# Optimization experiments

Hardware: AMD Instinct MI355X
Metric: run time of the kernel (lower is better)

Reference implementation:

```python
import jax, jax.numpy as jnp
import numpy as np

NEG_SLOPE = 0.2

def gat_conv(x, edge_index, W, a_src, a_dst, b, heads, out_ch, concat):
    # PyG GATConv with add_self_loops=True, LeakyReLU(0.2) attention.
    N = x.shape[0]
    loop = jnp.arange(N, dtype=edge_index.dtype)
    src = jnp.concatenate([edge_index[0], loop])  # source nodes j
    dst = jnp.concatenate([edge_index[1], loop])  # target nodes i
    h = (x @ W).reshape(N, heads, out_ch)                      # [N,H,C]
    alpha_src = jnp.sum(h * a_src[None], axis=-1)              # [N,H]
    alpha_dst = jnp.sum(h * a_dst[None], axis=-1)              # [N,H]
    e = alpha_src[src] + alpha_dst[dst]                        # [E,H]
    e = jax.nn.leaky_relu(e, NEG_SLOPE)
    # per-destination segment softmax (self-loops guarantee every segment non-empty)
    emax = jax.ops.segment_max(e, dst, num_segments=N)         # [N,H]
    ez = jnp.exp(e - emax[dst])
    denom = jax.ops.segment_sum(ez, dst, num_segments=N)       # [N,H]
    alpha = ez / denom[dst]                                    # [E,H]
    msg = h[src] * alpha[:, :, None]                           # [E,H,C]
    out = jax.ops.segment_sum(msg, dst, num_segments=N)        # [N,H,C]
    out = out.reshape(N, heads * out_ch) if concat else out.mean(axis=1)
    return out + b


def setup_inputs() -> dict:
    key = jax.random.key(0)
    ks = jax.random.split(key, 10)
    N, E = 100000, 3200000
    x = jax.random.normal(ks[0], (N, 7), dtype=jnp.float32)
    edge_index = jax.random.randint(ks[1], (2, E), 0, N, dtype=jnp.int32)
    W1 = jax.random.normal(ks[2], (7, 64), dtype=jnp.float32) * 0.3
    a_src1 = jax.random.normal(ks[3], (4, 16), dtype=jnp.float32) * 0.3
    a_dst1 = jax.random.normal(ks[4], (4, 16), dtype=jnp.float32) * 0.3
    b1 = jax.random.normal(ks[5], (64,), dtype=jnp.float32) * 0.1
    W2 = jax.random.normal(ks[6], (64, 6), dtype=jnp.float32) * 0.15
    a_src2 = jax.random.normal(ks[7], (1, 6), dtype=jnp.float32) * 0.3
    a_dst2 = jax.random.normal(ks[8], (1, 6), dtype=jnp.float32) * 0.3
    b2 = jax.random.normal(ks[9], (6,), dtype=jnp.float32) * 0.1
    return {"x": x, "edge_index": edge_index, "W1": W1, "a_src1": a_src1,
            "a_dst1": a_dst1, "b1": b1, "W2": W2, "a_src2": a_src2,
            "a_dst2": a_dst2, "b2": b2}


def reference(x, edge_index, W1, a_src1, a_dst1, b1, W2, a_src2, a_dst2, b2):
    h = gat_conv(x, edge_index, W1, a_src1, a_dst1, b1, heads=4, out_ch=16, concat=True)
    h = jax.nn.elu(h)
    h = gat_conv(h, edge_index, W2, a_src2, a_dst2, b2, heads=1, out_ch=6, concat=True)
    return jax.nn.log_softmax(h, axis=1)
```

## Files before the change

kernel.cpp:

```cpp
#include <hip/hip_runtime.h>
#include <math.h>

#define NEG_SLOPE 0.2f

__device__ __forceinline__ float lrelu(float x) { return x > 0.f ? x : NEG_SLOPE * x; }

__device__ __forceinline__ unsigned encf(float f) {
    unsigned u = __float_as_uint(f);
    return (u & 0x80000000u) ? ~u : (u | 0x80000000u);
}
__device__ __forceinline__ float decf(unsigned u) {
    return __uint_as_float((u & 0x80000000u) ? (u ^ 0x80000000u) : ~u);
}

__global__ void __launch_bounds__(512)
phaseAH(const float* __restrict__ x, const float* __restrict__ W1,
        const float* __restrict__ a_src, const float* __restrict__ a_dst,
        const int* __restrict__ dst,
        float* __restrict__ xa, float* __restrict__ adst1,
        float* __restrict__ eloop1,
        int* __restrict__ counts, unsigned* __restrict__ gmax1,
        int N, int E, int nbuck) {
    __shared__ int hist[1024];
    __shared__ unsigned bmax1[4];
    int tid = threadIdx.x;
    for (int j = tid; j < nbuck; j += 512) hist[j] = 0;
    if (tid < 4) bmax1[tid] = 0u;
    __syncthreads();

    int per = (E + gridDim.x - 1) / gridDim.x;
    int i0 = blockIdx.x * per, i1 = min(E, i0 + per);
    for (int i = i0 + tid; i < i1; i += 512)
        atomicAdd(&hist[dst[i] >> 7], 1);

    int npb = (N + gridDim.x - 1) / gridDim.x;
    int n0 = blockIdx.x * npb, n1 = min(N, n0 + npb);
    int lane = tid & 63;
    int head = lane >> 4, c = lane & 15;
    for (int node = n0 + (tid >> 6); node < n1; node += 8) {
        float h = 0.f;
        #pragma unroll
        for (int k = 0; k < 7; k++) h += x[node * 7 + k] * W1[k * 64 + lane];

        float s = h * a_src[lane];
        float d = h * a_dst[lane];
        #pragma unroll
        for (int m = 8; m >= 1; m >>= 1) {
            s += __shfl_xor(s, m);
            d += __shfl_xor(d, m);
        }
        if (lane < 7) xa[(size_t)node * 12 + lane] = x[node * 7 + lane];
        if (c == 0) {
            xa[(size_t)node * 12 + 7 + head] = s;
            adst1[node * 4 + head] = d;
            eloop1[node * 4 + head] = lrelu(s + d);
            atomicMax(&bmax1[head], encf(s));
        }
    }
    __syncthreads();
    for (int j = tid; j < nbuck; j += 512)
        counts[j * gridDim.x + blockIdx.x] = hist[j];
    if (tid < 4) atomicMax(&gmax1[tid], bmax1[tid]);
}

__global__ void scan1(const int* __restrict__ in, int* __restrict__ outv,
                      int* __restrict__ blockSum, int n) {
    __shared__ int sm[256];
    int tid = threadIdx.x;
    int i = blockIdx.x * 256 + tid;
    int v = (i < n) ? in[i] : 0;
    sm[tid] = v;
    __syncthreads();
    for (int off = 1; off < 256; off <<= 1) {
        int t = sm[tid];
        int add = (tid >= off) ? sm[tid - off] : 0;
        __syncthreads();
        sm[tid] = t + add;
        __syncthreads();
    }
    if (i < n) outv[i] = sm[tid] - v;
    if (tid == 255) blockSum[blockIdx.x] = sm[255];
}

__global__ void scan2(int* __restrict__ blockSum, int nb) {
    __shared__ int sm[1024];
    int tid = threadIdx.x;
    int v = (tid < nb) ? blockSum[tid] : 0;
    sm[tid] = v;
    __syncthreads();
    for (int off = 1; off < 1024; off <<= 1) {
        int t = sm[tid];
        int add = (tid >= off) ? sm[tid - off] : 0;
        __syncthreads();
        sm[tid] = t + add;
        __syncthreads();
    }
    if (tid < nb) blockSum[tid] = sm[tid] - v;
}

__global__ void scatterS(const int* __restrict__ src, const int* __restrict__ dst,
                         const int* __restrict__ ocounts, const int* __restrict__ blockSum,
                         int* __restrict__ ebuf, int E, int nbuck) {
    __shared__ int cur[1024];
    for (int j = threadIdx.x; j < nbuck; j += blockDim.x) {
        int idx = j * gridDim.x + blockIdx.x;
        cur[j] = ocounts[idx] + blockSum[idx >> 8];
    }
    __syncthreads();
    int per = (E + gridDim.x - 1) / gridDim.x;
    int i0 = blockIdx.x * per, i1 = min(E, i0 + per);
    for (int i = i0 + threadIdx.x; i < i1; i += blockDim.x) {
        int d = dst[i];
        int b = d >> 7;
        int pos = atomicAdd(&cur[b], 1);
        ebuf[pos] = src[i] | ((d & 127) << 17);
    }
}

__global__ void __launch_bounds__(512, 2)
fusedG1(const int* __restrict__ ebuf, const int* __restrict__ ocounts,
        const int* __restrict__ blockSum, const unsigned* __restrict__ gmax1,
        const float* __restrict__ xa, const float* __restrict__ adst1,
        const float* __restrict__ eloop1,
        const float* __restrict__ W1, const float* __restrict__ b1,
        const float* __restrict__ W2,
        const float* __restrict__ a_src2, const float* __restrict__ a_dst2,
        int* __restrict__ rowstart, int* __restrict__ deg, int* __restrict__ csr,
        float* __restrict__ h2pad, float* __restrict__ asrc2,
        float* __restrict__ adst2, float* __restrict__ eloop2,
        unsigned* __restrict__ gmax2, int N, int E, int G, int nbuck) {
    int b = blockIdx.x;
    int idxb = b * G;
    int beg = ocounts[idxb] + blockSum[idxb >> 8];
    int end = E;
    if (b + 1 < nbuck) {
        int idx2 = (b + 1) * G;
        end = ocounts[idx2] + blockSum[idx2 >> 8];
    }
    int base = b << 7;
    int tid = threadIdx.x;

    __shared__ int cnt[128], sc[128], rloc[128], lcur[128];
    __shared__ float W1s[448], W2s[384], b1s[64];
    __shared__ unsigned bmax2s;

    if (tid == 0) bmax2s = 0u;
    if (tid < 128) cnt[tid] = 0;
    for (int j = tid; j < 448; j += 512) W1s[j] = W1[j];
    for (int j = tid; j < 384; j += 512) W2s[j] = W2[j];
    if (tid < 64) b1s[tid] = b1[tid];
    __syncthreads();
    for (int i = beg + tid; i < end; i += 512)
        atomicAdd(&cnt[ebuf[i] >> 17], 1);
    __syncthreads();
    if (tid < 128) sc[tid] = cnt[tid];
    __syncthreads();
    for (int off = 1; off < 128; off <<= 1) {
        int t = (tid < 128) ? sc[tid] : 0;
        int add = (tid >= off && tid < 128) ? sc[tid - off] : 0;
        __syncthreads();
        if (tid < 128) sc[tid] = t + add;
        __syncthreads();
    }
    if (tid < 128) {
        int ex = sc[tid] - cnt[tid];
        rloc[tid] = beg + ex;
        lcur[tid] = 0;
        int node = base + tid;
        if (node < N) { rowstart[node] = beg + ex; deg[node] = cnt[tid]; }
    }
    __syncthreads();
    for (int i = beg + tid; i < end; i += 512) {
        int e = ebuf[i];
        int j = e >> 17;
        int pos = atomicAdd(&lcur[j], 1);
        csr[rloc[j] + pos] = e & 0x1FFFF;
    }
    __syncthreads();

    int g = tid >> 2, h = tid & 3;
    int node = base + g;
    if (node < N) {
        int grs = rloc[g], dg = cnt[g];
        float adh = adst1[node * 4 + h];
        float m = lrelu(decf(gmax1[h]) + adh);
        float z0 = __expf(eloop1[node * 4 + h] - m);
        float den = z0;

        const float4* xav = (const float4*)xa;
        float4 S0 = xav[(size_t)node * 3];
        float4 S1 = xav[(size_t)node * 3 + 1];
        float xc0 = z0 * S0.x, xc1 = z0 * S0.y, xc2 = z0 * S0.z, xc3 = z0 * S0.w;
        float xc4 = z0 * S1.x, xc5 = z0 * S1.y, xc6 = z0 * S1.z;

        if (dg > 0) {
            int iB = (dg > 1) ? 1 : 0;
            int sA = csr[grs];
            int sB = csr[grs + iB];
            float4 A0 = xav[(size_t)sA * 3], A1 = xav[(size_t)sA * 3 + 1], A2 = xav[(size_t)sA * 3 + 2];
            float4 B0 = xav[(size_t)sB * 3], B1 = xav[(size_t)sB * 3 + 1], B2 = xav[(size_t)sB * 3 + 2];
            for (int k = 0; k < dg; ++k) {
                int k2 = (k + 2 < dg) ? k + 2 : dg - 1;
                int sC = csr[grs + k2];
                float4 C0 = xav[(size_t)sC * 3], C1 = xav[(size_t)sC * 3 + 1], C2 = xav[(size_t)sC * 3 + 2];
                float av = (h == 0) ? A1.w : (h == 1) ? A2.x : (h == 2) ? A2.y : A2.z;
                float z = __expf(lrelu(av + adh) - m);
                den += z;
                xc0 = fmaf(z, A0.x, xc0); xc1 = fmaf(z, A0.y, xc1);
                xc2 = fmaf(z, A0.z, xc2); xc3 = fmaf(z, A0.w, xc3);
                xc4 = fmaf(z, A1.x, xc4); xc5 = fmaf(z, A1.y, xc5);
                xc6 = fmaf(z, A1.z, xc6);
                A0 = B0; A1 = B1; A2 = B2;
                B0 = C0; B1 = C1; B2 = C2;
            }
        }

        float inv = 1.f / den;
        float xv0 = xc0 * inv, xv1 = xc1 * inv, xv2 = xc2 * inv, xv3 = xc3 * inv;
        float xv4 = xc4 * inv, xv5 = xc5 * inv, xv6 = xc6 * inv;
        float hh[6] = {0.f, 0.f, 0.f, 0.f, 0.f, 0.f};
        #pragma unroll
        for (int c = 0; c < 16; ++c) {
            int ch = h * 16 + c;
            const float* Wc = &W1s[ch];
            float v = xv0 * Wc[0] + xv1 * Wc[64] + xv2 * Wc[128] + xv3 * Wc[192]
                    + xv4 * Wc[256] + xv5 * Wc[320] + xv6 * Wc[384] + b1s[ch];
            v = v > 0.f ? v : __expf(v) - 1.f;
            const float* W2c = &W2s[ch * 6];
            #pragma unroll
            for (int c2 = 0; c2 < 6; ++c2) hh[c2] = fmaf(v, W2c[c2], hh[c2]);
        }
        #pragma unroll
        for (int c2 = 0; c2 < 6; ++c2) {
            hh[c2] += __shfl_xor(hh[c2], 1);
            hh[c2] += __shfl_xor(hh[c2], 2);
        }
        float as = 0.f, ad = 0.f;
        #pragma unroll
        for (int c2 = 0; c2 < 6; ++c2) {
            as += hh[c2] * a_src2[c2];
            ad += hh[c2] * a_dst2[c2];
        }
        if (h == 0) {
            #pragma unroll
            for (int c2 = 0; c2 < 6; ++c2) h2pad[(size_t)node * 8 + c2] = hh[c2];
            h2pad[(size_t)node * 8 + 6] = as;
            asrc2[node] = as;
            adst2[node] = ad;
            eloop2[node] = lrelu(as + ad);
            atomicMax(&bmax2s, encf(as));
        }
    }
    __syncthreads();
    if (tid == 0) atomicMax(gmax2, bmax2s);
}

__global__ void gatherL2(const int* __restrict__ csr, const int* __restrict__ rowstart,
                         const int* __restrict__ deg, const unsigned* __restrict__ gmax2,
                         const float* __restrict__ h2pad, const float* __restrict__ adst2,
                         const float* __restrict__ eloop2,
                         const float* __restrict__ b2, float* __restrict__ out, int N) {
    int node = blockIdx.x * 8 + (threadIdx.x >> 5);
    if (node >= N) return;
    int lane = threadIdx.x & 31;
    int rs = rowstart[node], ke = rs + deg[node];

    float adn = adst2[node];
    float m = lrelu(decf(*gmax2) + adn);

    float den = 0.f;
    float a0 = 0.f, a1 = 0.f, a2 = 0.f, a3 = 0.f, a4 = 0.f, a5 = 0.f;
    if (lane == 0) {
        float z0 = __expf(eloop2[node] - m);
        den = z0;
        float4 lo = ((const float4*)h2pad)[(size_t)node * 2];
        float4 hi = ((const float4*)h2pad)[(size_t)node * 2 + 1];
        a0 = z0 * lo.x; a1 = z0 * lo.y; a2 = z0 * lo.z;
        a3 = z0 * lo.w; a4 = z0 * hi.x; a5 = z0 * hi.y;
    }
    for (int k = rs + lane; k < ke; k += 32) {
        int s = csr[k];
        float4 lo = ((const float4*)h2pad)[(size_t)s * 2];
        float4 hi = ((const float4*)h2pad)[(size_t)s * 2 + 1];
        float z = __expf(lrelu(hi.z + adn) - m);
        den += z;
        a0 = fmaf(z, lo.x, a0); a1 = fmaf(z, lo.y, a1); a2 = fmaf(z, lo.z, a2);
        a3 = fmaf(z, lo.w, a3); a4 = fmaf(z, hi.x, a4); a5 = fmaf(z, hi.y, a5);
    }
    #pragma unroll
    for (int mm = 16; mm >= 1; mm >>= 1) {
        den += __shfl_xor(den, mm);
        a0 += __shfl_xor(a0, mm); a1 += __shfl_xor(a1, mm); a2 += __shfl_xor(a2, mm);
        a3 += __shfl_xor(a3, mm); a4 += __shfl_xor(a4, mm); a5 += __shfl_xor(a5, mm);
    }
    if (lane == 0) {
        float inv = 1.f / den;
        float v[6] = { a0 * inv + b2[0], a1 * inv + b2[1], a2 * inv + b2[2],
                       a3 * inv + b2[3], a4 * inv + b2[4], a5 * inv + b2[5] };
        float mxv = -1e30f;
        #pragma unroll
        for (int cc = 0; cc < 6; cc++) mxv = fmaxf(mxv, v[cc]);
        float ssum = 0.f;
        #pragma unroll
        for (int cc = 0; cc < 6; cc++) ssum += __expf(v[cc] - mxv);
        float lse = mxv + logf(ssum);
        #pragma unroll
        for (int cc = 0; cc < 6; cc++) out[node * 6 + cc] = v[cc] - lse;
    }
}

extern "C" void kernel_launch(void* const* d_in, const int* in_sizes, int n_in,
                              void* d_out, int out_size, void* d_ws, size_t ws_size,
                              hipStream_t stream) {
    const float* x      = (const float*)d_in[0];
    const int*   ei     = (const int*)d_in[1];
    const float* W1     = (const float*)d_in[2];
    const float* a_src1 = (const float*)d_in[3];
    const float* a_dst1 = (const float*)d_in[4];
    const float* b1     = (const float*)d_in[5];
    const float* W2     = (const float*)d_in[6];
    const float* a_src2 = (const float*)d_in[7];
    const float* a_dst2 = (const float*)d_in[8];
    const float* b2     = (const float*)d_in[9];
    float* out = (float*)d_out;

    const int N = in_sizes[0] / 7;
    const int E = in_sizes[1] / 2;
    const int* src = ei;
    const int* dst = ei + E;
    const int nbuck = (N + 127) >> 7;
    const int G = 256;
    const int M = nbuck * G;

    float* w = (float*)d_ws;
    float* xa     = w;  w += (size_t)N * 12;
    float* adst1  = w;  w += (size_t)N * 4;
    float* eloop1 = w;  w += (size_t)N * 4;
    float* h2pad  = w;  w += (size_t)N * 8;
    float* asrc2  = w;  w += (size_t)N;
    float* adst2  = w;  w += (size_t)N;
    float* eloop2 = w;  w += (size_t)N;
    int* ip = (int*)w;
    int* ebuf     = ip; ip += E;
    int* deg      = ip; ip += N;
    int* rowstart = ip; ip += N;
    int* blockSum = ip; ip += 1024;
    int* csr      = ip; ip += E;
    int* counts   = ip; ip += M;
    int* ocounts  = ip; ip += M;
    unsigned* gmax1 = (unsigned*)ip; ip += 4;
    unsigned* gmax2 = (unsigned*)ip; ip += 4;

    int nbM = (M + 255) / 256;

    hipMemsetAsync(gmax1, 0, 8 * sizeof(unsigned), stream);
    phaseAH<<<dim3(G), 512, 0, stream>>>(x, W1, a_src1, a_dst1, dst,
                                         xa, adst1, eloop1,
                                         counts, gmax1, N, E, nbuck);
    scan1<<<dim3(nbM), 256, 0, stream>>>(counts, ocounts, blockSum, M);
    scan2<<<1, 1024, 0, stream>>>(blockSum, nbM);
    scatterS<<<dim3(G), 512, 0, stream>>>(src, dst, ocounts, blockSum, ebuf, E, nbuck);
    fusedG1<<<dim3(nbuck), 512, 0, stream>>>(ebuf, ocounts, blockSum, gmax1,
                                             xa, adst1, eloop1,
                                             W1, b1, W2, a_src2, a_dst2,
                                             rowstart, deg, csr,
                                             h2pad, asrc2, adst2, eloop2,
                                             gmax2, N, E, G, nbuck);
    gatherL2<<<dim3((N + 7) / 8), 256, 0, stream>>>(csr, rowstart, deg, gmax2,
                                                    h2pad, adst2, eloop2, b2, out, N);
}
```

Measured before the change: 210.9 us.

## Widen dst buckets to 256 nodes and assign two heads per thread in fusedG1

Destination buckets now cover 256 nodes instead of 128, which halves the number of fusedG1 blocks and of histogram/scatter bins. In fusedG1 each thread now handles two attention heads for one node instead of one, so each gathered neighbour row of xa is loaded by half as many threads. This trades more registers per thread (two sets of accumulators) and a serial loop over twice as many edges per block for less redundant gather traffic. The blockSum indexing is simplified to blockSum[b], which relies on G equal to 256.

```diff
diff --git a/kernel.cpp b/kernel.cpp
--- a/kernel.cpp
+++ b/kernel.cpp
@@ -21,7 +21,7 @@
         float* __restrict__ eloop1,
         int* __restrict__ counts, unsigned* __restrict__ gmax1,
         int N, int E, int nbuck) {
-    __shared__ int hist[1024];
+    __shared__ int hist[512];
     __shared__ unsigned bmax1[4];
     int tid = threadIdx.x;
     for (int j = tid; j < nbuck; j += 512) hist[j] = 0;
@@ -31,7 +31,7 @@
     int per = (E + gridDim.x - 1) / gridDim.x;
     int i0 = blockIdx.x * per, i1 = min(E, i0 + per);
     for (int i = i0 + tid; i < i1; i += 512)
-        atomicAdd(&hist[dst[i] >> 7], 1);
+        atomicAdd(&hist[dst[i] >> 8], 1);
 
     int npb = (N + gridDim.x - 1) / gridDim.x;
     int n0 = blockIdx.x * npb, n1 = min(N, n0 + npb);
@@ -101,7 +101,7 @@
 __global__ void scatterS(const int* __restrict__ src, const int* __restrict__ dst,
                          const int* __restrict__ ocounts, const int* __restrict__ blockSum,
                          int* __restrict__ ebuf, int E, int nbuck) {
-    __shared__ int cur[1024];
+    __shared__ int cur[512];
     for (int j = threadIdx.x; j < nbuck; j += blockDim.x) {
         int idx = j * gridDim.x + blockIdx.x;
         cur[j] = ocounts[idx] + blockSum[idx >> 8];
@@ -111,9 +111,9 @@
     int i0 = blockIdx.x * per, i1 = min(E, i0 + per);
     for (int i = i0 + threadIdx.x; i < i1; i += blockDim.x) {
         int d = dst[i];
-        int b = d >> 7;
+        int b = d >> 8;
         int pos = atomicAdd(&cur[b], 1);
-        ebuf[pos] = src[i] | ((d & 127) << 17);
+        ebuf[pos] = src[i] | ((d & 255) << 17);
     }
 }
 
@@ -130,22 +130,18 @@
         float* __restrict__ adst2, float* __restrict__ eloop2,
         unsigned* __restrict__ gmax2, int N, int E, int G, int nbuck) {
     int b = blockIdx.x;
-    int idxb = b * G;
-    int beg = ocounts[idxb] + blockSum[idxb >> 8];
+    int beg = ocounts[b * G] + blockSum[b];
     int end = E;
-    if (b + 1 < nbuck) {
-        int idx2 = (b + 1) * G;
-        end = ocounts[idx2] + blockSum[idx2 >> 8];
-    }
-    int base = b << 7;
+    if (b + 1 < nbuck) end = ocounts[(b + 1) * G] + blockSum[b + 1];
+    int base = b << 8;
     int tid = threadIdx.x;
 
-    __shared__ int cnt[128], sc[128], rloc[128], lcur[128];
+    __shared__ int cnt[256], sc[256], rloc[256], lcur[256];
     __shared__ float W1s[448], W2s[384], b1s[64];
     __shared__ unsigned bmax2s;
 
     if (tid == 0) bmax2s = 0u;
-    if (tid < 128) cnt[tid] = 0;
+    if (tid < 256) cnt[tid] = 0;
     for (int j = tid; j < 448; j += 512) W1s[j] = W1[j];
     for (int j = tid; j < 384; j += 512) W2s[j] = W2[j];
     if (tid < 64) b1s[tid] = b1[tid];
@@ -153,16 +149,16 @@
     for (int i = beg + tid; i < end; i += 512)
         atomicAdd(&cnt[ebuf[i] >> 17], 1);
     __syncthreads();
-    if (tid < 128) sc[tid] = cnt[tid];
-    __syncthreads();
-    for (int off = 1; off < 128; off <<= 1) {
-        int t = (tid < 128) ? sc[tid] : 0;
-        int add = (tid >= off && tid < 128) ? sc[tid - off] : 0;
-        __syncthreads();
-        if (tid < 128) sc[tid] = t + add;
-        __syncthreads();
-    }
-    if (tid < 128) {
+    if (tid < 256) sc[tid] = cnt[tid];
+    __syncthreads();
+    for (int off = 1; off < 256; off <<= 1) {
+        int t = (tid < 256) ? sc[tid] : 0;
+        int add = (tid >= off && tid < 256) ? sc[tid - off] : 0;
+        __syncthreads();
+        if (tid < 256) sc[tid] = t + add;
+        __syncthreads();
+    }
+    if (tid < 256) {
         int ex = sc[tid] - cnt[tid];
         rloc[tid] = beg + ex;
         lcur[tid] = 0;
@@ -178,20 +174,26 @@
     }
     __syncthreads();
 
-    int g = tid >> 2, h = tid & 3;
+    int g = tid >> 1, hp = tid & 1;
     int node = base + g;
     if (node < N) {
         int grs = rloc[g], dg = cnt[g];
-        float adh = adst1[node * 4 + h];
-        float m = lrelu(decf(gmax1[h]) + adh);
-        float z0 = __expf(eloop1[node * 4 + h] - m);
-        float den = z0;
+        int hA = hp * 2, hB = hA + 1;
+        float adhA = adst1[node * 4 + hA];
+        float adhB = adst1[node * 4 + hB];
+        float mA = lrelu(decf(gmax1[hA]) + adhA);
+        float mB = lrelu(decf(gmax1[hB]) + adhB);
+        float z0A = __expf(eloop1[node * 4 + hA] - mA);
+        float z0B = __expf(eloop1[node * 4 + hB] - mB);
+        float denA = z0A, denB = z0B;
 
         const float4* xav = (const float4*)xa;
         float4 S0 = xav[(size_t)node * 3];
         float4 S1 = xav[(size_t)node * 3 + 1];
-        float xc0 = z0 * S0.x, xc1 = z0 * S0.y, xc2 = z0 * S0.z, xc3 = z0 * S0.w;
-        float xc4 = z0 * S1.x, xc5 = z0 * S1.y, xc6 = z0 * S1.z;
+        float aA0 = z0A * S0.x, aA1 = z0A * S0.y, aA2 = z0A * S0.z, aA3 = z0A * S0.w;
+        float aA4 = z0A * S1.x, aA5 = z0A * S1.y, aA6 = z0A * S1.z;
+        float aB0 = z0B * S0.x, aB1 = z0B * S0.y, aB2 = z0B * S0.z, aB3 = z0B * S0.w;
+        float aB4 = z0B * S1.x, aB5 = z0B * S1.y, aB6 = z0B * S1.z;
 
         if (dg > 0) {
             int iB = (dg > 1) ? 1 : 0;
@@ -203,45 +205,64 @@
                 int k2 = (k + 2 < dg) ? k + 2 : dg - 1;
                 int sC = csr[grs + k2];
                 float4 C0 = xav[(size_t)sC * 3], C1 = xav[(size_t)sC * 3 + 1], C2 = xav[(size_t)sC * 3 + 2];
-                float av = (h == 0) ? A1.w : (h == 1) ? A2.x : (h == 2) ? A2.y : A2.z;
-                float z = __expf(lrelu(av + adh) - m);
-                den += z;
-                xc0 = fmaf(z, A0.x, xc0); xc1 = fmaf(z, A0.y, xc1);
-                xc2 = fmaf(z, A0.z, xc2); xc3 = fmaf(z, A0.w, xc3);
-                xc4 = fmaf(z, A1.x, xc4); xc5 = fmaf(z, A1.y, xc5);
-                xc6 = fmaf(z, A1.z, xc6);
+                float avA = hp ? A2.y : A1.w;
+                float avB = hp ? A2.z : A2.x;
+                float zA = __expf(lrelu(avA + adhA) - mA);
+                float zB = __expf(lrelu(avB + adhB) - mB);
+                denA += zA; denB += zB;
+                aA0 = fmaf(zA, A0.x, aA0); aA1 = fmaf(zA, A0.y, aA1);
+                aA2 = fmaf(zA, A0.z, aA2); aA3 = fmaf(zA, A0.w, aA3);
+                aA4 = fmaf(zA, A1.x, aA4); aA5 = fmaf(zA, A1.y, aA5);
+                aA6 = fmaf(zA, A1.z, aA6);
+                aB0 = fmaf(zB, A0.x, aB0); aB1 = fmaf(zB, A0.y, aB1);
+                aB2 = fmaf(zB, A0.z, aB2); aB3 = fmaf(zB, A0.w, aB3);
+                aB4 = fmaf(zB, A1.x, aB4); aB5 = fmaf(zB, A1.y, aB5);
+                aB6 = fmaf(zB, A1.z, aB6);
                 A0 = B0; A1 = B1; A2 = B2;
                 B0 = C0; B1 = C1; B2 = C2;
             }
         }
 
-        float inv = 1.f / den;
-        float xv0 = xc0 * inv, xv1 = xc1 * inv, xv2 = xc2 * inv, xv3 = xc3 * inv;
-        float xv4 = xc4 * inv, xv5 = xc5 * inv, xv6 = xc6 * inv;
+        float invA = 1.f / denA, invB = 1.f / denB;
+        float xvA[7] = { aA0 * invA, aA1 * invA, aA2 * invA, aA3 * invA,
+                         aA4 * invA, aA5 * invA, aA6 * invA };
+        float xvB[7] = { aB0 * invB, aB1 * invB, aB2 * invB, aB3 * invB,
+                         aB4 * invB, aB5 * invB, aB6 * invB };
         float hh[6] = {0.f, 0.f, 0.f, 0.f, 0.f, 0.f};
         #pragma unroll
         for (int c = 0; c < 16; ++c) {
-            int ch = h * 16 + c;
+            int ch = hA * 16 + c;
             const float* Wc = &W1s[ch];
-            float v = xv0 * Wc[0] + xv1 * Wc[64] + xv2 * Wc[128] + xv3 * Wc[192]
-                    + xv4 * Wc[256] + xv5 * Wc[320] + xv6 * Wc[384] + b1s[ch];
+            float v = xvA[0] * Wc[0] + xvA[1] * Wc[64] + xvA[2] * Wc[128]
+                    + xvA[3] * Wc[192] + xvA[4] * Wc[256] + xvA[5] * Wc[320]
+                    + xvA[6] * Wc[384] + b1s[ch];
             v = v > 0.f ? v : __expf(v) - 1.f;
             const float* W2c = &W2s[ch * 6];
             #pragma unroll
             for (int c2 = 0; c2 < 6; ++c2) hh[c2] = fmaf(v, W2c[c2], hh[c2]);
         }
         #pragma unroll
-        for (int c2 = 0; c2 < 6; ++c2) {
-            hh[c2] += __shfl_xor(hh[c2], 1);
-            hh[c2] += __shfl_xor(hh[c2], 2);
-        }
+        for (int c = 0; c < 16; ++c) {
+            int ch = hB * 16 + c;
+            const float* Wc = &W1s[ch];
+            float v = xvB[0] * Wc[0] + xvB[1] * Wc[64] + xvB[2] * Wc[128]
+                    + xvB[3] * Wc[192] + xvB[4] * Wc[256] + xvB[5] * Wc[320]
+                    + xvB[6] * Wc[384] + b1s[ch];
+            v = v > 0.f ? v : __expf(v) - 1.f;
+            const float* W2c = &W2s[ch * 6];
+            #pragma unroll
+            for (int c2 = 0; c2 < 6; ++c2) hh[c2] = fmaf(v, W2c[c2], hh[c2]);
+        }
+        #pragma unroll
+        for (int c2 = 0; c2 < 6; ++c2) hh[c2] += __shfl_xor(hh[c2], 1);
+
         float as = 0.f, ad = 0.f;
         #pragma unroll
         for (int c2 = 0; c2 < 6; ++c2) {
             as += hh[c2] * a_src2[c2];
             ad += hh[c2] * a_dst2[c2];
         }
-        if (h == 0) {
+        if (hp == 0) {
             #pragma unroll
             for (int c2 = 0; c2 < 6; ++c2) h2pad[(size_t)node * 8 + c2] = hh[c2];
             h2pad[(size_t)node * 8 + 6] = as;
@@ -328,7 +349,7 @@
     const int E = in_sizes[1] / 2;
     const int* src = ei;
     const int* dst = ei + E;
-    const int nbuck = (N + 127) >> 7;
+    const int nbuck = (N + 255) >> 8;
     const int G = 256;
     const int M = nbuck * G;
 
```

Measured after the change: 215.9 us. 2.4% more time.
